# Kernel optimization log

Hardware: AMD Instinct MI355X
Metric: run time of the kernel (lower is better)

## Reference

```python
import jax, jax.numpy as jnp
import numpy as np

CODEBOOK_NUM = 2
CENTROIDS_NUM = 256
CENTROID_LEN = 4
BLOCK_SIZE = 64
ROWS = 8192
COLUMNS = 8192


def setup_inputs() -> dict:
    key = jax.random.key(0)
    k1, k2, k3 = jax.random.split(key, 3)
    numel = ROWS * COLUMNS
    codebooks = jax.random.normal(k1, (CODEBOOK_NUM, CENTROIDS_NUM, CENTROID_LEN), dtype=jnp.float32)
    # scales are per-block L2 norms in the original -> strictly positive
    scales = jax.random.uniform(k2, (numel // BLOCK_SIZE, 1), dtype=jnp.float32, minval=0.5, maxval=1.5)
    codes = jax.random.randint(k3, (CODEBOOK_NUM, numel // CENTROID_LEN // CODEBOOK_NUM), 0, CENTROIDS_NUM, dtype=jnp.int64 if jax.config.jax_enable_x64 else jnp.int32)
    return {"codebooks": codebooks, "scales": scales, "codes": codes, "rows": ROWS, "columns": COLUMNS}


def reference(codebooks, scales, codes, rows, columns):
    # differentiable_dequantize:
    #   codes[i] += centroids_num * i ; flatten codebooks to [codebook_num*centroids_num, centroid_len]
    #   embedding_bag with consecutive offsets == plain gather of centroid vectors
    codebook_num, centroids_num, centroid_len = codebooks.shape
    offset = (jnp.arange(codebook_num, dtype=codes.dtype) * centroids_num)[:, None]
    flat_codes = (codes + offset).reshape(-1)                      # [numel/centroid_len]
    flat_cb = codebooks.reshape(codebook_num * centroids_num, centroid_len)
    rec = jnp.take(flat_cb, flat_codes, axis=0)                    # [numel/centroid_len, centroid_len]
    n_blocks = scales.shape[0]
    out = rec.reshape(n_blocks, -1) * scales                       # [numel/block_size, block_size]
    return out.reshape(rows, columns)
```

## Files before the change

kernel.cpp:

```cpp
#include <hip/hip_runtime.h>


#define N_GROUPS  16777216
#define HALF      8388608

__global__ __launch_bounds__(256) void dequant_kernel(
    const float* __restrict__ codebooks,
    const float* __restrict__ scales,
    const int*   __restrict__ codes,
    float*       __restrict__ out)
{
    const int i = blockIdx.x * blockDim.x + threadIdx.x;

    const int code = codes[i];

    const int cb_off = (i >= HALF) ? 256 : 0;

    const float4 cent = ((const float4*)codebooks)[cb_off + code];

    const float s = scales[i >> 4];

    float4 o;
    o.x = cent.x * s;
    o.y = cent.y * s;
    o.z = cent.z * s;
    o.w = cent.w * s;

    ((float4*)out)[i] = o;
}

extern "C" void kernel_launch(void* const* d_in, const int* in_sizes, int n_in,
                              void* d_out, int out_size, void* d_ws, size_t ws_size,
                              hipStream_t stream) {
    const float* codebooks = (const float*)d_in[0];
    const float* scales    = (const float*)d_in[1];
    const int*   codes     = (const int*)d_in[2];
    float*       out       = (float*)d_out;

    dequant_kernel<<<N_GROUPS / 256, 256, 0, stream>>>(codebooks, scales, codes, out);
}
```

Before: 329.5 us.

## Stage codebook in LDS, process 8 groups per thread with nontemporal IO

Each block now loads its half's 256-entry codebook into shared memory and gathers centroids from LDS instead of global memory. Each thread handles 8 groups, issuing all code and scale loads up front before computing, and uses nontemporal loads and stores for the streaming data. This aims to cut gather traffic through cache and increase memory-level parallelism, at the cost of a barrier per block and fewer blocks.

After: 322.5 us. 1.02x faster.

```diff
diff --git a/kernel.cpp b/kernel.cpp
--- a/kernel.cpp
+++ b/kernel.cpp
@@ -3,39 +3,53 @@
 
 #define N_GROUPS  16777216
 #define HALF      8388608
+#define GPT       8
+#define BLOCK     256
+#define GROUPS_PER_BLOCK (BLOCK * GPT)
+
+typedef float f32x4 __attribute__((ext_vector_type(4)));
 
 __global__ __launch_bounds__(256) void dequant_kernel(
-    const float* __restrict__ codebooks,
+    const f32x4* __restrict__ codebooks,
     const float* __restrict__ scales,
     const int*   __restrict__ codes,
-    float*       __restrict__ out)
+    f32x4*       __restrict__ out)
 {
-    const int i = blockIdx.x * blockDim.x + threadIdx.x;
+    __shared__ f32x4 lut[256];
 
-    const int code = codes[i];
+    const int base = blockIdx.x * GROUPS_PER_BLOCK;
+    const int half = (base >= HALF) ? 256 : 0;
 
-    const int cb_off = (i >= HALF) ? 256 : 0;
+    lut[threadIdx.x] = codebooks[half + threadIdx.x];
+    __syncthreads();
 
-    const float4 cent = ((const float4*)codebooks)[cb_off + code];
+    int   code[GPT];
+    float s[GPT];
 
-    const float s = scales[i >> 4];
+    #pragma unroll
+    for (int k = 0; k < GPT; ++k) {
+        const int g = base + k * BLOCK + threadIdx.x;
+        code[k] = __builtin_nontemporal_load(&codes[g]);
+        s[k]    = __builtin_nontemporal_load(&scales[g >> 4]);
+    }
 
-    float4 o;
-    o.x = cent.x * s;
-    o.y = cent.y * s;
-    o.z = cent.z * s;
-    o.w = cent.w * s;
-
-    ((float4*)out)[i] = o;
+    #pragma unroll
+    for (int k = 0; k < GPT; ++k) {
+        const int g = base + k * BLOCK + threadIdx.x;
+        f32x4 c = lut[code[k]];
+        c *= s[k];
+        __builtin_nontemporal_store(c, &out[g]);
+    }
 }
 
 extern "C" void kernel_launch(void* const* d_in, const int* in_sizes, int n_in,
                               void* d_out, int out_size, void* d_ws, size_t ws_size,
                               hipStream_t stream) {
-    const float* codebooks = (const float*)d_in[0];
+    const f32x4* codebooks = (const f32x4*)d_in[0];
     const float* scales    = (const float*)d_in[1];
     const int*   codes     = (const int*)d_in[2];
-    float*       out       = (float*)d_out;
+    f32x4*       out       = (f32x4*)d_out;
 
-    dequant_kernel<<<N_GROUPS / 256, 256, 0, stream>>>(codebooks, scales, codes, out);
+    dequant_kernel<<<N_GROUPS / GROUPS_PER_BLOCK, BLOCK, 0, stream>>>(
+        codebooks, scales, codes, out);
 }
```
